# Performance work log

Hardware: AMD Instinct MI355X
Metric: run time of the kernel (lower is better)

## Reference

```python
import jax, jax.numpy as jnp
import numpy as np

DIM = 2048
N_HEADS = 16
HEAD_DIM = DIM // N_HEADS
ROPE_BASE = 10000


def l2norm(x, axis=-1, eps=1e-12):
    n = jnp.sqrt(jnp.sum(x * x, axis=axis, keepdims=True))
    return x / jnp.maximum(n, eps)


def rope_tables(T, dim, base, dtype):
    theta = 1.0 / (base ** (jnp.arange(0, dim, 2, dtype=dtype) / dim))  # [dim/2]
    ang = jnp.arange(T, dtype=dtype)[:, None] * theta[None, :]          # [T, dim/2]
    return jnp.sin(ang), jnp.cos(ang)


def apply_rope(x, sin, cos):
    # x: [B, H, T, D]; sin/cos: [T, D/2] (half-split convention, not interleaved)
    half = x.shape[-1] // 2
    xr, xi = x[..., :half], x[..., half:]
    yr = xr * cos - xi * sin
    yi = xr * sin + xi * cos
    return jnp.concatenate([yr, yi], axis=-1)


def setup_inputs() -> dict:
    key = jax.random.key(0)
    ks = jax.random.split(key, 5)
    B, T = 1, 2048
    x = jax.random.normal(ks[0], (B, T, DIM), dtype=jnp.float32)
    wq = jax.random.normal(ks[1], (DIM, DIM), dtype=jnp.float32) * 0.02
    wk = jax.random.normal(ks[2], (DIM, DIM), dtype=jnp.float32) * 0.02
    wv = jax.random.normal(ks[3], (DIM, DIM), dtype=jnp.float32) * 0.02
    wo = jax.random.normal(ks[4], (DIM, DIM), dtype=jnp.float32) * 0.02
    sqk = jnp.ones((N_HEADS, 1, HEAD_DIM), dtype=jnp.float32) * (1.0 / DIM ** 0.5)
    return {"x": x, "wq": wq, "wk": wk, "wv": wv, "wo": wo, "sqk": sqk}


def reference(x, wq, wk, wv, wo, sqk):
    B, T, C = x.shape
    H, D = N_HEADS, HEAD_DIM
    restore = C ** 0.5  # restore_scale_sqk = sqkinit / sqkscale
    actual_sqk = sqk * restore  # [H, 1, D]

    def proj(w):
        return jnp.einsum('btc,oc->bto', x, w).reshape(B, T, H, D).transpose(0, 2, 1, 3)

    q = proj(wq)  # [B, H, T, D]
    new_k = proj(wk)
    new_v = proj(wv)

    sin, cos = rope_tables(T, D, ROPE_BASE, x.dtype)
    q = apply_rope(q, sin, cos) * actual_sqk
    k = apply_rope(new_k, sin, cos) * actual_sqk

    # NOTE: original uses scale=head_dim**0.5 (multiplies by sqrt(D))
    scores = jnp.einsum('bhqd,bhkd->bhqk', q, k) * (D ** 0.5)
    mask = jnp.tril(jnp.ones((T, T), dtype=bool))
    scores = jnp.where(mask, scores, jnp.finfo(scores.dtype).min)
    attn = jax.nn.softmax(scores, axis=-1)
    out = jnp.einsum('bhqk,bhkd->bhqd', attn, new_v)  # [B, H, T, D]
    out = out.transpose(0, 2, 1, 3).reshape(B, T, C)
    out = jnp.einsum('btc,oc->bto', out, wo)
    return (l2norm(out), (new_k, new_v))
```

## Files before the change

kernel.cpp:

```cpp
#include <hip/hip_runtime.h>

typedef __bf16 bf16x8 __attribute__((ext_vector_type(8)));
typedef float f32x4 __attribute__((ext_vector_type(4)));
typedef unsigned short us4 __attribute__((ext_vector_type(4)));

constexpr int TT = 2048;
constexpr int CC = 2048;
constexpr int HH = 16;
constexpr int DD = 128;

__device__ __forceinline__ unsigned short f2bf(float f) {
  unsigned u = __builtin_bit_cast(unsigned, f);
  u += 0x7FFFu + ((u >> 16) & 1u);
  return (unsigned short)(u >> 16);
}
__device__ __forceinline__ float bf2f(unsigned short b) {
  unsigned u = ((unsigned)b) << 16;
  return __builtin_bit_cast(float, u);
}

__device__ __forceinline__ void gld_lds16(const unsigned short* g, unsigned short* l) {
  __builtin_amdgcn_global_load_lds(
      (const __attribute__((address_space(1))) unsigned int*)g,
      (__attribute__((address_space(3))) unsigned int*)l,
      16, 0, 0);
}

__device__ __forceinline__ int soff(int qt) {
  int g = qt >> 2, rem = qt & 3;
  return (g + 1) * (2 * g + rem);
}

__global__ __launch_bounds__(256) void k_cvt5(
    const float* __restrict__ s0, const float* __restrict__ s1,
    const float* __restrict__ s2, const float* __restrict__ s3,
    const float* __restrict__ s4,
    unsigned short* __restrict__ d0, unsigned short* __restrict__ d1,
    unsigned short* __restrict__ d2, unsigned short* __restrict__ d3,
    unsigned short* __restrict__ d4) {
  const int m = blockIdx.y;
  const float* src = (m == 0) ? s0 : (m == 1) ? s1 : (m == 2) ? s2 : (m == 3) ? s3 : s4;
  unsigned short* dst = (m == 0) ? d0 : (m == 1) ? d1 : (m == 2) ? d2 : (m == 3) ? d3 : d4;
  int i = blockIdx.x * 256 + threadIdx.x;
  const float4* s = (const float4*)src;
  float4 a = s[2 * i], b = s[2 * i + 1];
  us4 lo = { f2bf(a.x), f2bf(a.y), f2bf(a.z), f2bf(a.w) };
  us4 hi = { f2bf(b.x), f2bf(b.y), f2bf(b.z), f2bf(b.w) };
  us4* d = (us4*)dst;
  d[2 * i] = lo;
  d[2 * i + 1] = hi;
}

template <int MODE>
__global__ __launch_bounds__(512, 2) void k_gemm8p(
    const unsigned short* __restrict__ A, const unsigned short* __restrict__ B,
    int N, int K, int kspan,
    float* __restrict__ out0, float* __restrict__ out1,
    float* __restrict__ out2, float* __restrict__ out3) {
  __shared__ alignas(16) unsigned short As[2][2][128 * 64];
  __shared__ alignas(16) unsigned short Bs[2][2][128 * 64];
  const int tid = threadIdx.x;
  const int m0 = blockIdx.y * 256, n0 = blockIdx.x * 256;
  const int kbeg = blockIdx.z * kspan;
  const int NT = kspan >> 6, NT2 = NT >> 1;
  const int wid = tid >> 6, lane = tid & 63;
  const int wr = wid >> 2, wc = wid & 3;
  const int lr = lane & 15, lg = lane >> 4;
  const int bh = wc >> 1, brow0 = (wc & 1) * 64;

  const int sr0 = tid >> 3, sc0 = tid & 7;
  const unsigned short* Ab = A + kbeg;
  const unsigned short* Bb = B + kbeg;

  auto stageA = [&](int buf, int half, int tile) {
    const int koff = tile * 64;
#pragma unroll
    for (int j = 0; j < 2; ++j) {
      const int r = sr0 + j * 64;
      gld_lds16(Ab + (size_t)(m0 + half * 128 + r) * K + koff + ((sc0 ^ (r & 7)) * 8),
                &As[buf][half][(tid + j * 512) * 8]);
    }
  };
  auto stageB = [&](int buf, int half, int tile) {
    const int koff = tile * 64;
#pragma unroll
    for (int j = 0; j < 2; ++j) {
      const int r = sr0 + j * 64;
      gld_lds16(Bb + (size_t)(n0 + half * 128 + r) * K + koff + ((sc0 ^ (r & 7)) * 8),
                &Bs[buf][half][(tid + j * 512) * 8]);
    }
  };

  f32x4 acc[8][4] = {};
  bf16x8 alo[4][2], ahi[4][2], ba[2][2], bb[2][2];

  auto rdAlo = [&](int d) {
#pragma unroll
    for (int im = 0; im < 4; ++im)
#pragma unroll
      for (int kk = 0; kk < 2; ++kk) {
        const int row = im * 16 + lr;
        alo[im][kk] = *(const bf16x8*)(&As[d][wr][row * 64 + (((kk * 4 + lg) ^ (row & 7)) * 8)]);
      }
  };
  auto rdAhi = [&](int d) {
#pragma unroll
    for (int im = 0; im < 4; ++im)
#pragma unroll
      for (int kk = 0; kk < 2; ++kk) {
        const int row = (4 + im) * 16 + lr;
        ahi[im][kk] = *(const bf16x8*)(&As[d][wr][row * 64 + (((kk * 4 + lg) ^ (row & 7)) * 8)]);
      }
  };
  auto rdBa = [&](int d) {
#pragma unroll
    for (int in = 0; in < 2; ++in)
#pragma unroll
      for (int kk = 0; kk < 2; ++kk) {
        const int row = brow0 + in * 16 + lr;
        ba[in][kk] = *(const bf16x8*)(&Bs[d][bh][row * 64 + (((kk * 4 + lg) ^ (row & 7)) * 8)]);
      }
  };
  auto rdBb = [&](int d) {
#pragma unroll
    for (int in = 0; in < 2; ++in)
#pragma unroll
      for (int kk = 0; kk < 2; ++kk) {
        const int row = brow0 + (2 + in) * 16 + lr;
        bb[in][kk] = *(const bf16x8*)(&Bs[d][bh][row * 64 + (((kk * 4 + lg) ^ (row & 7)) * 8)]);
      }
  };

#define MFMA_Q(MB, NB, AF, BF)                                                     \
  __builtin_amdgcn_s_setprio(1);                                                   \
  _Pragma("unroll") for (int im = 0; im < 4; ++im)                                 \
      _Pragma("unroll") for (int in = 0; in < 2; ++in)                             \
          _Pragma("unroll") for (int kk = 0; kk < 2; ++kk)                         \
              acc[MB + im][NB + in] = __builtin_amdgcn_mfma_f32_16x16x32_bf16(     \
                  AF[im][kk], BF[in][kk], acc[MB + im][NB + in], 0, 0, 0);         \
  __builtin_amdgcn_s_setprio(0);

#define WAIT_LGKM0                                      \
  asm volatile("s_waitcnt lgkmcnt(0)" ::: "memory");    \
  __builtin_amdgcn_sched_barrier(0);
#define BAR __builtin_amdgcn_s_barrier();

  stageB(0, 0, 0); stageB(0, 1, 0); stageA(0, 0, 0); stageA(0, 1, 0);
  if (NT > 1) { stageB(1, 0, 1); stageB(1, 1, 1); }
  asm volatile("s_waitcnt vmcnt(4)" ::: "memory");
  __builtin_amdgcn_sched_barrier(0);
  BAR

  for (int t = 0; t < NT2; ++t) {
    const int t1 = 2 * t + 1, t2 = 2 * t + 2, t3 = 2 * t + 3;
    const bool s2 = t2 < NT, s3 = t3 < NT;

    rdAlo(0); rdBa(0);
    stageA(1, 0, t1);
    BAR WAIT_LGKM0
    MFMA_Q(0, 0, alo, ba)
    BAR

    rdBb(0);
    stageA(1, 1, t1);
    BAR WAIT_LGKM0
    MFMA_Q(0, 2, alo, bb)
    BAR

    rdAhi(0);
    if (s2) stageB(0, 0, t2);
    BAR WAIT_LGKM0
    MFMA_Q(4, 2, ahi, bb)
    BAR

    if (s2) stageB(0, 1, t2);
    MFMA_Q(4, 0, ahi, ba)
    if (s2) { asm volatile("s_waitcnt vmcnt(4)" ::: "memory"); }
    else    { asm volatile("s_waitcnt vmcnt(0)" ::: "memory"); }
    __builtin_amdgcn_sched_barrier(0);
    BAR

    rdAlo(1); rdBa(1);
    if (s2) stageA(0, 0, t2);
    BAR WAIT_LGKM0
    MFMA_Q(0, 0, alo, ba)
    BAR

    rdBb(1);
    if (s2) stageA(0, 1, t2);
    BAR WAIT_LGKM0
    MFMA_Q(0, 2, alo, bb)
    BAR

    rdAhi(1);
    if (s3) stageB(1, 0, t3);
    BAR WAIT_LGKM0
    MFMA_Q(4, 2, ahi, bb)
    BAR

    if (s3) stageB(1, 1, t3);
    MFMA_Q(4, 0, ahi, ba)
    if (s3) { asm volatile("s_waitcnt vmcnt(4)" ::: "memory"); }
    else    { asm volatile("s_waitcnt vmcnt(0)" ::: "memory"); }
    __builtin_amdgcn_sched_barrier(0);
    BAR
  }
#undef MFMA_Q
#undef WAIT_LGKM0
#undef BAR

  float* dst = out0;
  if (MODE == 1) {
    int z = blockIdx.z;
    dst = (z == 0) ? out0 : (z == 1) ? out1 : (z == 2) ? out2 : out3;
  }
#pragma unroll
  for (int mf = 0; mf < 8; ++mf) {
    const int row = m0 + wr * 128 + mf * 16 + lg * 4;
#pragma unroll
    for (int nf = 0; nf < 4; ++nf) {
      const int col = n0 + wc * 64 + nf * 16 + lr;
#pragma unroll
      for (int r = 0; r < 4; ++r) {
        float v = acc[mf][nf][r];
        int rr = row + r;
        if (MODE == 0) {
          if (col < 2048) {
            out0[(size_t)rr * 2048 + col] = v;
          } else if (col < 4096) {
            int c = col - 2048;
            out1[(size_t)(c >> 7) * (TT * DD) + (size_t)rr * DD + (c & 127)] = v;
          } else {
            int c = col - 4096;
            out2[(size_t)(c >> 7) * (TT * DD) + (size_t)rr * DD + (c & 127)] = v;
          }
        } else {
          dst[(size_t)rr * N + col] = v;
        }
      }
    }
  }
}

__global__ __launch_bounds__(256) void k_rope(
    const float* __restrict__ Qf, const float* __restrict__ Kraw,
    const float* __restrict__ sqk,
    unsigned short* __restrict__ qb, unsigned short* __restrict__ kb) {
  const int t = blockIdx.x;
  for (int i = threadIdx.x; i < HH * 64; i += 256) {
    int h = i >> 6, dp = i & 63;
    float theta = expf(-(float)dp * 0.14391156831212787f);
    float ang = (float)t * theta;
    float sn, cs;
    sincosf(ang, &sn, &cs);
    float qr = Qf[(size_t)t * CC + h * DD + dp];
    float qi = Qf[(size_t)t * CC + h * DD + dp + 64];
    const float* kp = Kraw + (size_t)h * TT * DD + (size_t)t * DD;
    float kr = kp[dp], ki = kp[dp + 64];
    float sr = sqk[h * DD + dp];
    float si = sqk[h * DD + dp + 64];
    float qsr = sr * 512.0f, qsi = si * 512.0f;
    float ksr = sr * 45.25483399593904f, ksi = si * 45.25483399593904f;
    unsigned short* qo = qb + ((size_t)h * TT + t) * DD;
    unsigned short* ko = kb + ((size_t)h * TT + t) * DD;
    qo[dp]      = f2bf((qr * cs - qi * sn) * qsr);
    qo[dp + 64] = f2bf((qr * sn + qi * cs) * qsi);
    ko[dp]      = f2bf((kr * cs - ki * sn) * ksr);
    ko[dp + 64] = f2bf((kr * sn + ki * cs) * ksi);
  }
}

__global__ __launch_bounds__(256) void k_vt(
    const float* __restrict__ Vraw, unsigned short* __restrict__ vt) {
  const int h = blockIdx.z;
  const int t0 = blockIdx.x * 64, d0 = blockIdx.y * 64;
  __shared__ unsigned short tile[64][65];
  const float* vp = Vraw + (size_t)h * TT * DD;
  for (int i = threadIdx.x; i < 4096; i += 256) {
    int r = i >> 6, c = i & 63;
    tile[r][c] = f2bf(vp[(size_t)(t0 + r) * DD + d0 + c]);
  }
  __syncthreads();
  unsigned short* op = vt + (size_t)h * DD * TT;
  for (int i = threadIdx.x; i < 4096; i += 256) {
    int dr = i >> 6, tc = i & 63;
    op[(size_t)(d0 + dr) * TT + t0 + tc] = tile[tc][dr];
  }
}

__global__ __launch_bounds__(512) void k_attn_split(
    const unsigned short* __restrict__ qb, const unsigned short* __restrict__ kb,
    const unsigned short* __restrict__ vt,
    unsigned short* __restrict__ po, float* __restrict__ marr, float* __restrict__ larr) {
  const int qt = blockIdx.x, h = blockIdx.y, s = blockIdx.z;
  if (4 * s > qt) return;
  const int slot = h * 40 + soff(qt) + s;
  const int kbeg = 512 * s;
  const int kend = min(kbeg + 512, 128 * qt + 128);
  const int ntiles = (kend - kbeg) >> 6;
  const int tid = threadIdx.x;
  const int wid = tid >> 6, lane = tid & 63;
  const int lr = lane & 15, lg = lane >> 4;
  const int q0 = qt * 128 + wid * 16;

  __shared__ alignas(16) unsigned short Ks[64 * 128];
  __shared__ alignas(16) unsigned short Vs[128 * 64];
  __shared__ alignas(16) unsigned short P[8][16][72];

  const unsigned short* qh = qb + (size_t)h * TT * DD;
  const unsigned short* kh = kb + (size_t)h * TT * DD;
  const unsigned short* vh = vt + (size_t)h * DD * TT;

  bf16x8 qf[4];
#pragma unroll
  for (int c = 0; c < 4; ++c)
    qf[c] = *(const bf16x8*)(qh + (size_t)(q0 + lr) * DD + c * 32 + lg * 8);

  f32x4 acc[8] = {};
  float mrow[4] = {-3e38f, -3e38f, -3e38f, -3e38f};
  float lsum[4] = {0.f, 0.f, 0.f, 0.f};

  for (int kt = 0; kt < ntiles; ++kt) {
    const int k0 = kbeg + kt * 64;
#pragma unroll
    for (int half = 0; half < 2; ++half) {
      int ch = tid + half * 512;
      int r = ch >> 4, c4 = ch & 15;
      gld_lds16(kh + (size_t)(k0 + r) * DD + ((c4 ^ (r & 7)) * 8), Ks + ch * 8);
    }
#pragma unroll
    for (int half = 0; half < 2; ++half) {
      int ch = tid + half * 512;
      int d = ch >> 3, c8 = ch & 7;
      gld_lds16(vh + (size_t)d * TT + k0 + ((c8 ^ (d & 7)) * 8), Vs + ch * 8);
    }
    __syncthreads();

    if (k0 <= q0 + 15) {
      f32x4 sv[4] = {};
#pragma unroll
      for (int ktile = 0; ktile < 4; ++ktile) {
        const int row = ktile * 16 + lr;
#pragma unroll
        for (int c = 0; c < 4; ++c) {
          int chn = (c * 4 + lg) ^ (lr & 7);
          bf16x8 kf = *(const bf16x8*)(Ks + row * 128 + chn * 8);
          sv[ktile] = __builtin_amdgcn_mfma_f32_16x16x32_bf16(qf[c], kf, sv[ktile], 0, 0, 0);
        }
      }
      if (k0 + 63 > q0) {
#pragma unroll
        for (int ktile = 0; ktile < 4; ++ktile)
#pragma unroll
          for (int r = 0; r < 4; ++r) {
            int key = k0 + ktile * 16 + lr;
            int qrow = q0 + lg * 4 + r;
            if (key > qrow) sv[ktile][r] = -1e30f;
          }
      }
      float pmax[4];
#pragma unroll
      for (int r = 0; r < 4; ++r)
        pmax[r] = fmaxf(fmaxf(sv[0][r], sv[1][r]), fmaxf(sv[2][r], sv[3][r]));
#pragma unroll
      for (int msk = 1; msk <= 8; msk <<= 1)
#pragma unroll
        for (int r = 0; r < 4; ++r) pmax[r] = fmaxf(pmax[r], __shfl_xor(pmax[r], msk));
      float p[4][4], ps[4], scl[4];
#pragma unroll
      for (int r = 0; r < 4; ++r) {
        float mn = fmaxf(mrow[r], pmax[r]);
        scl[r] = __expf(mrow[r] - mn);
        mrow[r] = mn;
        ps[r] = 0.f;
#pragma unroll
        for (int ktile = 0; ktile < 4; ++ktile) {
          p[ktile][r] = __expf(sv[ktile][r] - mn);
          ps[r] += p[ktile][r];
        }
      }
#pragma unroll
      for (int msk = 1; msk <= 8; msk <<= 1)
#pragma unroll
        for (int r = 0; r < 4; ++r) ps[r] += __shfl_xor(ps[r], msk);
#pragma unroll
      for (int r = 0; r < 4; ++r) lsum[r] = lsum[r] * scl[r] + ps[r];
#pragma unroll
      for (int n = 0; n < 8; ++n)
#pragma unroll
        for (int r = 0; r < 4; ++r) acc[n][r] *= scl[r];
#pragma unroll
      for (int ktile = 0; ktile < 4; ++ktile)
#pragma unroll
        for (int r = 0; r < 4; ++r)
          P[wid][lg * 4 + r][ktile * 16 + lr] = f2bf(p[ktile][r]);
      asm volatile("s_waitcnt lgkmcnt(0)" ::: "memory");
      __builtin_amdgcn_sched_barrier(0);
      bf16x8 pf[2];
#pragma unroll
      for (int ks = 0; ks < 2; ++ks)
        pf[ks] = *(const bf16x8*)(&P[wid][lr][ks * 32 + lg * 8]);
#pragma unroll
      for (int n = 0; n < 8; ++n) {
        const int row = n * 16 + lr;
#pragma unroll
        for (int ks = 0; ks < 2; ++ks) {
          int chn = (ks * 4 + lg) ^ (lr & 7);
          bf16x8 vf = *(const bf16x8*)(Vs + row * 64 + chn * 8);
          acc[n] = __builtin_amdgcn_mfma_f32_16x16x32_bf16(pf[ks], vf, acc[n], 0, 0, 0);
        }
      }
    }
    __syncthreads();
  }

  unsigned short* pob = po + (size_t)slot * (128 * DD);
#pragma unroll
  for (int n = 0; n < 8; ++n)
#pragma unroll
    for (int r = 0; r < 4; ++r) {
      int row = wid * 16 + lg * 4 + r;
      pob[(size_t)row * DD + n * 16 + lr] = f2bf(acc[n][r]);
    }
  if (lr == 0) {
#pragma unroll
    for (int r = 0; r < 4; ++r) {
      int row = wid * 16 + lg * 4 + r;
      marr[(size_t)slot * 128 + row] = mrow[r];
      larr[(size_t)slot * 128 + row] = lsum[r];
    }
  }
}

__global__ __launch_bounds__(256) void k_attn_reduce(
    const unsigned short* __restrict__ po, const float* __restrict__ marr,
    const float* __restrict__ larr, unsigned short* __restrict__ ob) {
  const int qt = blockIdx.x, h = blockIdx.y;
  const int ns = (qt >> 2) + 1;
  const int sb = h * 40 + soff(qt);
  const int tid = threadIdx.x;
  const int row = tid >> 1, d0 = (tid & 1) * 64;
  float mstar = -3e38f;
  for (int s = 0; s < ns; ++s) mstar = fmaxf(mstar, marr[(size_t)(sb + s) * 128 + row]);
  float w[4];
  float ltot = 0.f;
  for (int s = 0; s < ns; ++s) {
    w[s] = __expf(marr[(size_t)(sb + s) * 128 + row] - mstar);
    ltot += w[s] * larr[(size_t)(sb + s) * 128 + row];
  }
  float inv = 1.0f / ltot;
  float o[64] = {};
  for (int s = 0; s < ns; ++s) {
    const bf16x8* pp = (const bf16x8*)(po + (size_t)(sb + s) * (128 * DD) + (size_t)row * DD + d0);
    float ws = w[s];
#pragma unroll
    for (int j = 0; j < 8; ++j) {
      bf16x8 v = pp[j];
#pragma unroll
      for (int e = 0; e < 8; ++e) o[j * 8 + e] += ws * (float)v[e];
    }
  }
  unsigned short* op = ob + (size_t)(qt * 128 + row) * CC + h * DD + d0;
#pragma unroll
  for (int j = 0; j < 16; ++j) {
    us4 t = { f2bf(o[4 * j] * inv), f2bf(o[4 * j + 1] * inv),
              f2bf(o[4 * j + 2] * inv), f2bf(o[4 * j + 3] * inv) };
    ((us4*)op)[j] = t;
  }
}

__global__ __launch_bounds__(256) void k_l2norm(
    const float* __restrict__ Of0, const float* __restrict__ Of1,
    const float* __restrict__ Of2, const float* __restrict__ Of3,
    float* __restrict__ out) {
  const int t = blockIdx.x;
  const int tid = threadIdx.x;
  const float4* p0 = (const float4*)(Of0 + (size_t)t * CC);
  const float4* p1 = (const float4*)(Of1 + (size_t)t * CC);
  const float4* p2 = (const float4*)(Of2 + (size_t)t * CC);
  const float4* p3 = (const float4*)(Of3 + (size_t)t * CC);
  float4 a = p0[2 * tid], b = p0[2 * tid + 1];
  float4 a1 = p1[2 * tid], b1 = p1[2 * tid + 1];
  float4 a2 = p2[2 * tid], b2 = p2[2 * tid + 1];
  float4 a3 = p3[2 * tid], b3 = p3[2 * tid + 1];
  a.x += a1.x + a2.x + a3.x; a.y += a1.y + a2.y + a3.y;
  a.z += a1.z + a2.z + a3.z; a.w += a1.w + a2.w + a3.w;
  b.x += b1.x + b2.x + b3.x; b.y += b1.y + b2.y + b3.y;
  b.z += b1.z + b2.z + b3.z; b.w += b1.w + b2.w + b3.w;
  float ss = a.x * a.x + a.y * a.y + a.z * a.z + a.w * a.w +
             b.x * b.x + b.y * b.y + b.z * b.z + b.w * b.w;
#pragma unroll
  for (int msk = 1; msk < 64; msk <<= 1) ss += __shfl_xor(ss, msk);
  __shared__ float red[4];
  if ((tid & 63) == 0) red[tid >> 6] = ss;
  __syncthreads();
  ss = red[0] + red[1] + red[2] + red[3];
  float sc = 1.0f / fmaxf(sqrtf(ss), 1e-12f);
  float4 oa = { a.x * sc, a.y * sc, a.z * sc, a.w * sc };
  float4 obv = { b.x * sc, b.y * sc, b.z * sc, b.w * sc };
  float4* o = (float4*)(out + (size_t)t * CC);
  o[2 * tid] = oa;
  o[2 * tid + 1] = obv;
}

extern "C" void kernel_launch(void* const* d_in, const int* in_sizes, int n_in,
                              void* d_out, int out_size, void* d_ws, size_t ws_size,
                              hipStream_t stream) {
  const float* x   = (const float*)d_in[0];
  const float* wq  = (const float*)d_in[1];
  const float* wk  = (const float*)d_in[2];
  const float* wv  = (const float*)d_in[3];
  const float* wo  = (const float*)d_in[4];
  const float* sqk = (const float*)d_in[5];

  float* out_norm = (float*)d_out;
  float* out_k = out_norm + (size_t)4 * 1024 * 1024;
  float* out_v = out_norm + (size_t)8 * 1024 * 1024;

  char* ws = (char*)d_ws;
  unsigned short* xb  = (unsigned short*)(ws);
  unsigned short* w1b = (unsigned short*)(ws + (8u << 20));
  unsigned short* wob = (unsigned short*)(ws + (32u << 20));
  unsigned short* qb  = (unsigned short*)(ws + (40u << 20));
  unsigned short* kb  = (unsigned short*)(ws + (48u << 20));
  unsigned short* vtb = (unsigned short*)(ws + (56u << 20));
  unsigned short* obb = (unsigned short*)(ws + (64u << 20));
  float* Qf = (float*)(ws + (72u << 20));

  unsigned short* po = (unsigned short*)(ws);
  float* marr = (float*)(ws + (22u << 20));
  float* larr = (float*)(ws + (23u << 20));

  float* Of0 = Qf;
  float* Of1 = (float*)(ws);
  float* Of2 = (float*)(ws + (16u << 20));
  float* Of3 = (float*)(ws + (40u << 20));

  k_cvt5<<<dim3(2048, 5), 256, 0, stream>>>(
      x, wq, wk, wv, wo,
      xb, w1b, w1b + (size_t)4 * 1024 * 1024, w1b + (size_t)8 * 1024 * 1024, wob);

  k_gemm8p<0><<<dim3(24, 8, 1), 512, 0, stream>>>(xb, w1b, 3 * CC, CC, CC,
                                                  Qf, out_k, out_v, nullptr);

  k_rope<<<TT, 256, 0, stream>>>(Qf, out_k, sqk, qb, kb);
  k_vt<<<dim3(32, 2, 16), 256, 0, stream>>>(out_v, vtb);

  k_attn_split<<<dim3(16, 16, 4), 512, 0, stream>>>(qb, kb, vtb, po, marr, larr);
  k_attn_reduce<<<dim3(16, 16), 256, 0, stream>>>(po, marr, larr, obb);

  k_gemm8p<1><<<dim3(8, 8, 4), 512, 0, stream>>>(obb, wob, CC, CC, CC / 4,
                                                 Of0, Of1, Of2, Of3);

  k_l2norm<<<TT, 256, 0, stream>>>(Of0, Of1, Of2, Of3, out_norm);
}
```

Before: 223.4 us.

## Retile QKV projection GEMM to 256x192 blocks and emit Q in bf16

Adds a dedicated QKV projection kernel with a 256x192 output tile, so the 6144-wide output splits into 256 blocks instead of 192. This spreads the work across more compute units and fills the device better. The Q projection is now stored as bf16 rather than fp32, which halves that intermediate's write and read traffic into the rope kernel. The cost is an extra rounding step on Q before rope is applied, and a narrower B tile that gives less reuse per block.

```diff
diff --git a/kernel.cpp b/kernel.cpp
--- a/kernel.cpp
+++ b/kernel.cpp
@@ -51,7 +51,207 @@
   d[2 * i + 1] = hi;
 }
 
-template <int MODE>
+#define WAIT_LGKM0                                      \
+  asm volatile("s_waitcnt lgkmcnt(0)" ::: "memory");    \
+  __builtin_amdgcn_sched_barrier(0);
+#define BAR __builtin_amdgcn_s_barrier();
+
+__global__ __launch_bounds__(512, 2) void k_gemm192(
+    const unsigned short* __restrict__ A, const unsigned short* __restrict__ B,
+    unsigned short* __restrict__ qraw,
+    float* __restrict__ outk, float* __restrict__ outv) {
+  __shared__ alignas(16) unsigned short As[2][256 * 64];
+  __shared__ alignas(16) unsigned short Bs[2][192 * 64];
+  const int K = CC, NT = K >> 6, NT2 = NT >> 1;
+  const int tid = threadIdx.x;
+  const int m0 = blockIdx.y * 256, n0 = blockIdx.x * 192;
+  const int wid = tid >> 6, lane = tid & 63;
+  const int wr = wid >> 2, wc = wid & 3;
+  const int lr = lane & 15, lg = lane >> 4;
+
+  auto stA = [&](int buf, int jb, int tile) {
+#pragma unroll
+    for (int j = jb; j < jb + 2; ++j) {
+      const int ch = tid + j * 512;
+      const int r = ch >> 3, c8 = ch & 7;
+      gld_lds16(A + (size_t)(m0 + r) * K + tile * 64 + ((c8 ^ (r & 7)) * 8),
+                &As[buf][ch * 8]);
+    }
+  };
+  auto stB2 = [&](int buf, int tile) {
+#pragma unroll
+    for (int j = 0; j < 2; ++j) {
+      const int ch = tid + j * 512;
+      const int r = ch >> 3, c8 = ch & 7;
+      gld_lds16(B + (size_t)(n0 + r) * K + tile * 64 + ((c8 ^ (r & 7)) * 8),
+                &Bs[buf][ch * 8]);
+    }
+  };
+  auto stB1 = [&](int buf, int tile) {
+    const int ch = tid + 1024;
+    const int r = ch >> 3, c8 = ch & 7;
+    gld_lds16(B + (size_t)(n0 + r) * K + tile * 64 + ((c8 ^ (r & 7)) * 8),
+              &Bs[buf][ch * 8]);
+  };
+
+  f32x4 acc[8][3] = {};
+  bf16x8 alo[4][2], ahi[4][2], b01[2][2], b2v[2];
+
+  auto rdAlo = [&](int d) {
+#pragma unroll
+    for (int im = 0; im < 4; ++im)
+#pragma unroll
+      for (int kk = 0; kk < 2; ++kk) {
+        const int row = wr * 128 + im * 16 + lr;
+        alo[im][kk] = *(const bf16x8*)(&As[d][row * 64 + (((kk * 4 + lg) ^ (row & 7)) * 8)]);
+      }
+  };
+  auto rdAhi = [&](int d) {
+#pragma unroll
+    for (int im = 0; im < 4; ++im)
+#pragma unroll
+      for (int kk = 0; kk < 2; ++kk) {
+        const int row = wr * 128 + (4 + im) * 16 + lr;
+        ahi[im][kk] = *(const bf16x8*)(&As[d][row * 64 + (((kk * 4 + lg) ^ (row & 7)) * 8)]);
+      }
+  };
+  auto rdB01 = [&](int d) {
+#pragma unroll
+    for (int in = 0; in < 2; ++in)
+#pragma unroll
+      for (int kk = 0; kk < 2; ++kk) {
+        const int row = wc * 48 + in * 16 + lr;
+        b01[in][kk] = *(const bf16x8*)(&Bs[d][row * 64 + (((kk * 4 + lg) ^ (row & 7)) * 8)]);
+      }
+  };
+  auto rdB2 = [&](int d) {
+#pragma unroll
+    for (int kk = 0; kk < 2; ++kk) {
+      const int row = wc * 48 + 32 + lr;
+      b2v[kk] = *(const bf16x8*)(&Bs[d][row * 64 + (((kk * 4 + lg) ^ (row & 7)) * 8)]);
+    }
+  };
+
+  auto q_lo01 = [&]() {
+    __builtin_amdgcn_s_setprio(1);
+#pragma unroll
+    for (int im = 0; im < 4; ++im)
+#pragma unroll
+      for (int in = 0; in < 2; ++in)
+#pragma unroll
+        for (int kk = 0; kk < 2; ++kk)
+          acc[im][in] = __builtin_amdgcn_mfma_f32_16x16x32_bf16(alo[im][kk], b01[in][kk], acc[im][in], 0, 0, 0);
+    __builtin_amdgcn_s_setprio(0);
+  };
+  auto q_lo2 = [&]() {
+    __builtin_amdgcn_s_setprio(1);
+#pragma unroll
+    for (int im = 0; im < 4; ++im)
+#pragma unroll
+      for (int kk = 0; kk < 2; ++kk)
+        acc[im][2] = __builtin_amdgcn_mfma_f32_16x16x32_bf16(alo[im][kk], b2v[kk], acc[im][2], 0, 0, 0);
+    __builtin_amdgcn_s_setprio(0);
+  };
+  auto q_hi2 = [&]() {
+    __builtin_amdgcn_s_setprio(1);
+#pragma unroll
+    for (int im = 0; im < 4; ++im)
+#pragma unroll
+      for (int kk = 0; kk < 2; ++kk)
+        acc[4 + im][2] = __builtin_amdgcn_mfma_f32_16x16x32_bf16(ahi[im][kk], b2v[kk], acc[4 + im][2], 0, 0, 0);
+    __builtin_amdgcn_s_setprio(0);
+  };
+  auto q_hi01 = [&]() {
+    __builtin_amdgcn_s_setprio(1);
+#pragma unroll
+    for (int im = 0; im < 4; ++im)
+#pragma unroll
+      for (int in = 0; in < 2; ++in)
+#pragma unroll
+        for (int kk = 0; kk < 2; ++kk)
+          acc[4 + im][in] = __builtin_amdgcn_mfma_f32_16x16x32_bf16(ahi[im][kk], b01[in][kk], acc[4 + im][in], 0, 0, 0);
+    __builtin_amdgcn_s_setprio(0);
+  };
+
+  stB2(0, 0); stB1(0, 0); stA(0, 0, 0); stA(0, 2, 0);
+  stB2(1, 1); stB1(1, 1);
+  asm volatile("s_waitcnt vmcnt(3)" ::: "memory");
+  __builtin_amdgcn_sched_barrier(0);
+  BAR
+
+  for (int t = 0; t < NT2; ++t) {
+    const int t1 = 2 * t + 1, t2 = 2 * t + 2, t3 = 2 * t + 3;
+    const bool s2 = t2 < NT;
+
+    rdAlo(0); rdB01(0);
+    stA(1, 0, t1);
+    BAR WAIT_LGKM0
+    q_lo01();
+    BAR
+    rdB2(0);
+    stA(1, 2, t1);
+    BAR WAIT_LGKM0
+    q_lo2();
+    BAR
+    rdAhi(0);
+    if (s2) stB2(0, t2);
+    BAR WAIT_LGKM0
+    q_hi2();
+    BAR
+    if (s2) stB1(0, t2);
+    q_hi01();
+    if (s2) { asm volatile("s_waitcnt vmcnt(3)" ::: "memory"); }
+    else    { asm volatile("s_waitcnt vmcnt(0)" ::: "memory"); }
+    __builtin_amdgcn_sched_barrier(0);
+    BAR
+
+    rdAlo(1); rdB01(1);
+    if (s2) stA(0, 0, t2);
+    BAR WAIT_LGKM0
+    q_lo01();
+    BAR
+    rdB2(1);
+    if (s2) stA(0, 2, t2);
+    BAR WAIT_LGKM0
+    q_lo2();
+    BAR
+    rdAhi(1);
+    if (s2) stB2(1, t3);
+    BAR WAIT_LGKM0
+    q_hi2();
+    BAR
+    if (s2) stB1(1, t3);
+    q_hi01();
+    if (s2) { asm volatile("s_waitcnt vmcnt(3)" ::: "memory"); }
+    else    { asm volatile("s_waitcnt vmcnt(0)" ::: "memory"); }
+    __builtin_amdgcn_sched_barrier(0);
+    BAR
+  }
+
+#pragma unroll
+  for (int mf = 0; mf < 8; ++mf) {
+    const int row = m0 + wr * 128 + mf * 16 + lg * 4;
+#pragma unroll
+    for (int nf = 0; nf < 3; ++nf) {
+      const int col = n0 + wc * 48 + nf * 16 + lr;
+#pragma unroll
+      for (int r = 0; r < 4; ++r) {
+        float v = acc[mf][nf][r];
+        int rr = row + r;
+        if (col < 2048) {
+          qraw[(size_t)rr * 2048 + col] = f2bf(v);
+        } else if (col < 4096) {
+          int c = col - 2048;
+          outk[(size_t)(c >> 7) * (TT * DD) + (size_t)rr * DD + (c & 127)] = v;
+        } else {
+          int c = col - 4096;
+          outv[(size_t)(c >> 7) * (TT * DD) + (size_t)rr * DD + (c & 127)] = v;
+        }
+      }
+    }
+  }
+}
+
 __global__ __launch_bounds__(512, 2) void k_gemm8p(
     const unsigned short* __restrict__ A, const unsigned short* __restrict__ B,
     int N, int K, int kspan,
@@ -140,11 +340,6 @@
                   AF[im][kk], BF[in][kk], acc[MB + im][NB + in], 0, 0, 0);         \
   __builtin_amdgcn_s_setprio(0);
 
-#define WAIT_LGKM0                                      \
-  asm volatile("s_waitcnt lgkmcnt(0)" ::: "memory");    \
-  __builtin_amdgcn_sched_barrier(0);
-#define BAR __builtin_amdgcn_s_barrier();
-
   stageB(0, 0, 0); stageB(0, 1, 0); stageA(0, 0, 0); stageA(0, 1, 0);
   if (NT > 1) { stageB(1, 0, 1); stageB(1, 1, 1); }
   asm volatile("s_waitcnt vmcnt(4)" ::: "memory");
@@ -160,19 +355,16 @@
     BAR WAIT_LGKM0
     MFMA_Q(0, 0, alo, ba)
     BAR
-
     rdBb(0);
     stageA(1, 1, t1);
     BAR WAIT_LGKM0
     MFMA_Q(0, 2, alo, bb)
     BAR
-
     rdAhi(0);
     if (s2) stageB(0, 0, t2);
     BAR WAIT_LGKM0
     MFMA_Q(4, 2, ahi, bb)
     BAR
-
     if (s2) stageB(0, 1, t2);
     MFMA_Q(4, 0, ahi, ba)
     if (s2) { asm volatile("s_waitcnt vmcnt(4)" ::: "memory"); }
@@ -185,19 +377,16 @@
     BAR WAIT_LGKM0
     MFMA_Q(0, 0, alo, ba)
     BAR
-
     rdBb(1);
     if (s2) stageA(0, 1, t2);
     BAR WAIT_LGKM0
     MFMA_Q(0, 2, alo, bb)
     BAR
-
     rdAhi(1);
     if (s3) stageB(1, 0, t3);
     BAR WAIT_LGKM0
     MFMA_Q(4, 2, ahi, bb)
     BAR
-
     if (s3) stageB(1, 1, t3);
     MFMA_Q(4, 0, ahi, ba)
     if (s3) { asm volatile("s_waitcnt vmcnt(4)" ::: "memory"); }
@@ -206,44 +395,27 @@
     BAR
   }
 #undef MFMA_Q
+
+  int z = blockIdx.z;
+  float* dst = (z == 0) ? out0 : (z == 1) ? out1 : (z == 2) ? out2 : out3;
+#pragma unroll
+  for (int mf = 0; mf < 8; ++mf) {
+    const int row = m0 + wr * 128 + mf * 16 + lg * 4;
+#pragma unroll
+    for (int nf = 0; nf < 4; ++nf) {
+      const int col = n0 + wc * 64 + nf * 16 + lr;
+#pragma unroll
+      for (int r = 0; r < 4; ++r) {
+        dst[(size_t)(row + r) * N + col] = acc[mf][nf][r];
+      }
+    }
+  }
+}
 #undef WAIT_LGKM0
 #undef BAR
 
-  float* dst = out0;
-  if (MODE == 1) {
-    int z = blockIdx.z;
-    dst = (z == 0) ? out0 : (z == 1) ? out1 : (z == 2) ? out2 : out3;
-  }
-#pragma unroll
-  for (int mf = 0; mf < 8; ++mf) {
-    const int row = m0 + wr * 128 + mf * 16 + lg * 4;
-#pragma unroll
-    for (int nf = 0; nf < 4; ++nf) {
-      const int col = n0 + wc * 64 + nf * 16 + lr;
-#pragma unroll
-      for (int r = 0; r < 4; ++r) {
-        float v = acc[mf][nf][r];
-        int rr = row + r;
-        if (MODE == 0) {
-          if (col < 2048) {
-            out0[(size_t)rr * 2048 + col] = v;
-          } else if (col < 4096) {
-            int c = col - 2048;
-            out1[(size_t)(c >> 7) * (TT * DD) + (size_t)rr * DD + (c & 127)] = v;
-          } else {
-            int c = col - 4096;
-            out2[(size_t)(c >> 7) * (TT * DD) + (size_t)rr * DD + (c & 127)] = v;
-          }
-        } else {
-          dst[(size_t)rr * N + col] = v;
-        }
-      }
-    }
-  }
-}
-
 __global__ __launch_bounds__(256) void k_rope(
-    const float* __restrict__ Qf, const float* __restrict__ Kraw,
+    const unsigned short* __restrict__ qraw, const float* __restrict__ Kraw,
     const float* __restrict__ sqk,
     unsigned short* __restrict__ qb, unsigned short* __restrict__ kb) {
   const int t = blockIdx.x;
@@ -253,8 +425,8 @@
     float ang = (float)t * theta;
     float sn, cs;
     sincosf(ang, &sn, &cs);
-    float qr = Qf[(size_t)t * CC + h * DD + dp];
-    float qi = Qf[(size_t)t * CC + h * DD + dp + 64];
+    float qr = bf2f(qraw[(size_t)t * CC + h * DD + dp]);
+    float qi = bf2f(qraw[(size_t)t * CC + h * DD + dp + 64]);
     const float* kp = Kraw + (size_t)h * TT * DD + (size_t)t * DD;
     float kr = kp[dp], ki = kp[dp + 64];
     float sr = sqk[h * DD + dp];
@@ -525,13 +697,13 @@
   unsigned short* kb  = (unsigned short*)(ws + (48u << 20));
   unsigned short* vtb = (unsigned short*)(ws + (56u << 20));
   unsigned short* obb = (unsigned short*)(ws + (64u << 20));
-  float* Qf = (float*)(ws + (72u << 20));
+  unsigned short* qraw = (unsigned short*)(ws + (72u << 20));
 
   unsigned short* po = (unsigned short*)(ws);
   float* marr = (float*)(ws + (22u << 20));
   float* larr = (float*)(ws + (23u << 20));
 
-  float* Of0 = Qf;
+  float* Of0 = (float*)(ws + (72u << 20));
   float* Of1 = (float*)(ws);
   float* Of2 = (float*)(ws + (16u << 20));
   float* Of3 = (float*)(ws + (40u << 20));
@@ -540,17 +712,16 @@
       x, wq, wk, wv, wo,
       xb, w1b, w1b + (size_t)4 * 1024 * 1024, w1b + (size_t)8 * 1024 * 1024, wob);
 
-  k_gemm8p<0><<<dim3(24, 8, 1), 512, 0, stream>>>(xb, w1b, 3 * CC, CC, CC,
-                                                  Qf, out_k, out_v, nullptr);
-
-  k_rope<<<TT, 256, 0, stream>>>(Qf, out_k, sqk, qb, kb);
+  k_gemm192<<<dim3(32, 8), 512, 0, stream>>>(xb, w1b, qraw, out_k, out_v);
+
+  k_rope<<<TT, 256, 0, stream>>>(qraw, out_k, sqk, qb, kb);
   k_vt<<<dim3(32, 2, 16), 256, 0, stream>>>(out_v, vtb);
 
   k_attn_split<<<dim3(16, 16, 4), 512, 0, stream>>>(qb, kb, vtb, po, marr, larr);
   k_attn_reduce<<<dim3(16, 16), 256, 0, stream>>>(po, marr, larr, obb);
 
-  k_gemm8p<1><<<dim3(8, 8, 4), 512, 0, stream>>>(obb, wob, CC, CC, CC / 4,
-                                                 Of0, Of1, Of2, Of3);
+  k_gemm8p<<<dim3(8, 8, 4), 512, 0, stream>>>(obb, wob, CC, CC, CC / 4,
+                                              Of0, Of1, Of2, Of3);
 
   k_l2norm<<<TT, 256, 0, stream>>>(Of0, Of1, Of2, Of3, out_norm);
 }
```

Measured after the change: 216.6 us. -3.1%, faster.
